# Kernel optimization log

Hardware: AMD Instinct MI355X
Metric: run time of the kernel (lower is better)

## Reference

```python
import jax, jax.numpy as jnp
import numpy as np

E = 768
H = 12
DK = E // H
B = 4
S = 2048
EPS = 1e-5


def setup_inputs() -> dict:
    key = jax.random.key(0)
    ks = jax.random.split(key, 8)
    # xavier_uniform bound for square [E, E] weight
    bound = float(np.sqrt(6.0 / (E + E)))
    def xavier(k):
        return jax.random.uniform(k, (E, E), jnp.float32, -bound, bound)
    return {
        "query": jax.random.normal(ks[0], (B, S, E), jnp.float32),
        "key": jax.random.normal(ks[1], (B, S, E), jnp.float32),
        "value": jax.random.normal(ks[2], (B, S, E), jnp.float32),
        "enc_attn_mask": jax.random.randint(ks[3], (B, S, S), 0, 2).astype(bool),
        "Wq": xavier(ks[4]),
        "Wk": xavier(ks[5]),
        "Wv": xavier(ks[6]),
        "Wo": xavier(ks[7]),
    }


def reference(query, key, value, enc_attn_mask, Wq, Wk, Wv, Wo):
    b, s, _ = query.shape
    # projections (nn.Linear: y = x @ W.T), split heads -> [b, h, s, dk]
    Q = (query @ Wq.T).reshape(b, s, H, DK).transpose(0, 2, 1, 3)
    K = (key @ Wk.T).reshape(b, s, H, DK).transpose(0, 2, 1, 3)
    V = (value @ Wv.T).reshape(b, s, H, DK).transpose(0, 2, 1, 3)
    # scaled dot-product attention with boolean mask (True -> -1e9)
    scores = jnp.einsum("bhqd,bhkd->bhqk", Q, K) / np.sqrt(DK).astype(np.float32)
    scores = jnp.where(enc_attn_mask[:, None, :, :], jnp.float32(-1e9), scores)
    attn = jax.nn.softmax(scores, axis=-1)
    context = jnp.einsum("bhqk,bhkd->bhqd", attn, V)
    context = context.transpose(0, 2, 1, 3).reshape(b, s, E)
    out = context @ Wo.T + query  # residual
    # fresh nn.LayerNorm(E): weight=1, bias=0, eps=1e-5
    mean = jnp.mean(out, axis=-1, keepdims=True)
    var = jnp.var(out, axis=-1, keepdims=True)
    return (out - mean) * jax.lax.rsqrt(var + EPS)
```

## Files before the change

### kernel.cpp

```cpp
#include <hip/hip_runtime.h>
#include <stdint.h>
#include <stddef.h>

#define HN   12
#define SN   2048
#define EN   768
#define DKN  64
#define BATCH 4
#define MROWS 8192

typedef short bf16x8 __attribute__((ext_vector_type(8)));
typedef float f32x4 __attribute__((ext_vector_type(4)));

__device__ __forceinline__ unsigned short f2bf(float f) {
  union { float f; unsigned u; } x; x.f = f;
  unsigned r = x.u + 0x7fffu + ((x.u >> 16) & 1u);
  return (unsigned short)(r >> 16);
}

#if __has_builtin(__builtin_amdgcn_cvt_pk_bf16_f32)
typedef __bf16 bf16v2 __attribute__((ext_vector_type(2)));
__device__ __forceinline__ unsigned pk_bf16(float a, float b) {
  union { bf16v2 v; unsigned u; } c;
  c.v = __builtin_amdgcn_cvt_pk_bf16_f32(a, b);
  return c.u;
}
#else
__device__ __forceinline__ unsigned pk_bf16(float a, float b) {
  return (unsigned)f2bf(a) | ((unsigned)f2bf(b) << 16);
}
#endif

#define GLD_LDS16(gptr, lptr) \
  __builtin_amdgcn_global_load_lds((const __attribute__((address_space(1))) void*)(gptr), \
                                   (__attribute__((address_space(3))) void*)(lptr), 16, 0, 0)

#define NBIG4 1572864
#define NW4   147456
__global__ __launch_bounds__(256) void cvt_all(const float* __restrict__ q,
                                               const float* __restrict__ k,
                                               const float* __restrict__ v,
                                               const float* __restrict__ wq,
                                               const float* __restrict__ wk,
                                               const float* __restrict__ wv,
                                               const float* __restrict__ wo,
                                               unsigned short* __restrict__ dst) {
  const int i = blockIdx.x * 256 + threadIdx.x;
  const float* src;
  int off;
  if (i < 3 * NBIG4) {
    const int r = i / NBIG4;
    src = (r == 0) ? q : (r == 1) ? k : v;
    off = i - r * NBIG4;
  } else {
    const int j = i - 3 * NBIG4;
    const int r = j / NW4;
    src = (r == 0) ? wq : (r == 1) ? wk : (r == 2) ? wv : wo;
    off = j - r * NW4;
  }
  float4 val = ((const float4*)src)[off];
  ushort4 o;
  o.x = f2bf(val.x); o.y = f2bf(val.y); o.z = f2bf(val.z); o.w = f2bf(val.w);
  ((ushort4*)dst)[i] = o;
}

__global__ __launch_bounds__(256) void mask_pack(const int* __restrict__ mask,
                                                 unsigned long long* __restrict__ out) {
  const int row = (blockIdx.x * 256 + threadIdx.x) >> 6;
  const int lane = threadIdx.x & 63;
  const int* mrow = mask + (size_t)row * SN;
  unsigned long long* orow = out + (size_t)row * 32;
  for (int kt = 0; kt < 32; ++kt) {
    int v = mrow[kt * 64 + lane];
    unsigned long long bm = __ballot(v != 0);
    if (lane == 0) orow[kt] = bm;
  }
}

__global__ __launch_bounds__(256) void gemm_qkv(const unsigned short* __restrict__ Xb,
                                                const unsigned short* __restrict__ Wb,
                                                unsigned short* __restrict__ Ob,
                                                float qscale) {
  __shared__ unsigned short As[128 * 32];
  __shared__ unsigned short Bs[128 * 32];
  const int tid  = threadIdx.x;
  const int wave = tid >> 6;
  const int lane = tid & 63;
  const int quad = lane >> 4;
  const int l16  = lane & 15;
  const int bm = blockIdx.x;
  const int bn = blockIdx.y;
  const int z  = blockIdx.z;
  const int wm = wave & 1;
  const int wn = wave >> 1;

  const unsigned short* X = Xb + (size_t)z * MROWS * EN;
  const unsigned short* W = Wb + (size_t)z * EN * EN;
  unsigned short* O = Ob + (size_t)z * MROWS * EN;

  f32x4 acc[4][4] = {};
  const int srow = lane >> 2;
  const int schk = lane & 3;

  for (int bk = 0; bk < 24; ++bk) {
    __syncthreads();
#pragma unroll
    for (int r = 0; r < 2; ++r) {
      const int rowblk = r * 64 + wave * 16;
      GLD_LDS16(X + (size_t)(bm * 128 + rowblk + srow) * EN + bk * 32 + schk * 8,
                As + rowblk * 32);
      GLD_LDS16(W + (size_t)(bn * 128 + rowblk + srow) * EN + bk * 32 + schk * 8,
                Bs + rowblk * 32);
    }
    __syncthreads();

    bf16x8 af[4], bfr[4];
#pragma unroll
    for (int mt = 0; mt < 4; ++mt)
      af[mt] = *(const bf16x8*)&As[(wm * 64 + mt * 16 + l16) * 32 + quad * 8];
#pragma unroll
    for (int nt = 0; nt < 4; ++nt)
      bfr[nt] = *(const bf16x8*)&Bs[(wn * 64 + nt * 16 + l16) * 32 + quad * 8];
#pragma unroll
    for (int mt = 0; mt < 4; ++mt)
#pragma unroll
      for (int nt = 0; nt < 4; ++nt)
        acc[mt][nt] = __builtin_amdgcn_mfma_f32_16x16x32_bf16(af[mt], bfr[nt], acc[mt][nt], 0, 0, 0);
  }

  const int m0 = bm * 128 + wm * 64;
  const int n0 = bn * 128 + wn * 64;
  const float scale = (z == 0) ? qscale : 1.0f;

  if (z < 2) {
#pragma unroll
    for (int mt = 0; mt < 4; ++mt) {
#pragma unroll
      for (int nt = 0; nt < 4; ++nt) {
        const int n = n0 + nt * 16 + l16;
        const int h = n >> 6, d = n & 63;
#pragma unroll
        for (int r = 0; r < 4; ++r) {
          const int m = m0 + mt * 16 + quad * 4 + r;
          const int b = m >> 11, s = m & 2047;
          O[((size_t)(b * HN + h) * SN + s) * DKN + d] = f2bf(acc[mt][nt][r] * scale);
        }
      }
    }
  } else {
#pragma unroll
    for (int mt = 0; mt < 4; ++mt) {
#pragma unroll
      for (int nt = 0; nt < 4; ++nt) {
        const int n = n0 + nt * 16 + l16;
        const int h = n >> 6, d = n & 63;
        const int m = m0 + mt * 16 + quad * 4;
        const int b = m >> 11, s = m & 2047;
        ushort4 pk;
        pk.x = f2bf(acc[mt][nt][0]);
        pk.y = f2bf(acc[mt][nt][1]);
        pk.z = f2bf(acc[mt][nt][2]);
        pk.w = f2bf(acc[mt][nt][3]);
        *(ushort4*)&O[((size_t)(b * HN + h) * DKN + d) * SN + s] = pk;
      }
    }
  }
}

__global__ __launch_bounds__(256) void gemm_out(const unsigned short* __restrict__ X,
                                                const unsigned short* __restrict__ W,
                                                float* __restrict__ O,
                                                const float* __restrict__ residual) {
  __shared__ unsigned short As[128 * 32];
  __shared__ unsigned short Bs[128 * 32];
  const int tid  = threadIdx.x;
  const int wave = tid >> 6;
  const int lane = tid & 63;
  const int quad = lane >> 4;
  const int l16  = lane & 15;
  const int bm = blockIdx.x;
  const int bn = blockIdx.y;
  const int wm = wave & 1;
  const int wn = wave >> 1;

  f32x4 acc[4][4] = {};
  const int srow = lane >> 2;
  const int schk = lane & 3;

  for (int bk = 0; bk < 24; ++bk) {
    __syncthreads();
#pragma unroll
    for (int r = 0; r < 2; ++r) {
      const int rowblk = r * 64 + wave * 16;
      GLD_LDS16(X + (size_t)(bm * 128 + rowblk + srow) * EN + bk * 32 + schk * 8,
                As + rowblk * 32);
      GLD_LDS16(W + (size_t)(bn * 128 + rowblk + srow) * EN + bk * 32 + schk * 8,
                Bs + rowblk * 32);
    }
    __syncthreads();

    bf16x8 af[4], bfr[4];
#pragma unroll
    for (int mt = 0; mt < 4; ++mt)
      af[mt] = *(const bf16x8*)&As[(wm * 64 + mt * 16 + l16) * 32 + quad * 8];
#pragma unroll
    for (int nt = 0; nt < 4; ++nt)
      bfr[nt] = *(const bf16x8*)&Bs[(wn * 64 + nt * 16 + l16) * 32 + quad * 8];
#pragma unroll
    for (int mt = 0; mt < 4; ++mt)
#pragma unroll
      for (int nt = 0; nt < 4; ++nt)
        acc[mt][nt] = __builtin_amdgcn_mfma_f32_16x16x32_bf16(af[mt], bfr[nt], acc[mt][nt], 0, 0, 0);
  }

  const int m0 = bm * 128 + wm * 64;
  const int n0 = bn * 128 + wn * 64;
#pragma unroll
  for (int mt = 0; mt < 4; ++mt) {
#pragma unroll
    for (int nt = 0; nt < 4; ++nt) {
      const int n = n0 + nt * 16 + l16;
#pragma unroll
      for (int r = 0; r < 4; ++r) {
        const int m = m0 + mt * 16 + quad * 4 + r;
        const size_t idx = (size_t)m * EN + n;
        O[idx] = acc[mt][nt][r] + residual[idx];
      }
    }
  }
}

__global__ __launch_bounds__(256, 4) void attn_kernel(const unsigned short* __restrict__ Q,
                                                      const unsigned short* __restrict__ K,
                                                      const unsigned short* __restrict__ Vt,
                                                      const unsigned* __restrict__ Mbits32,
                                                      unsigned short* __restrict__ Ctx) {
  __shared__ __align__(16) unsigned char LDSBUF[64 * 68 * 4];
  __shared__ float lpart[2][2][16];
  unsigned short* Ks = (unsigned short*)LDSBUF;
  unsigned short* Vs = (unsigned short*)(LDSBUF + 8192);
  float* Cmb = (float*)LDSBUF;

  const int tid  = threadIdx.x;
  const int wave = tid >> 6, lane = tid & 63;
  const int quad = lane >> 4, l16 = lane & 15;
  const int qhalf = wave >> 1, kh = wave & 1;
  const int qt = blockIdx.x, bh = blockIdx.y;
  const int b = bh / HN, h = bh - b * HN;

  const unsigned short* Qp = Q + (size_t)bh * SN * DKN;
  const unsigned short* Kp = K + (size_t)bh * SN * DKN;
  const unsigned short* Vp = Vt + (size_t)bh * DKN * SN;

  const int srow = lane >> 3;
  const int schk = lane & 7;
  const int swsrc = (schk ^ srow) * 8;
  const int c0 = (quad ^ (l16 & 7)) * 8;
  const int cv = (((kh << 2) + quad) ^ (l16 & 7)) * 8;
  const int shq = 31 - quad * 8;

  const int pw = wave * 8 + srow;
  const int yk = (((pw >> 2) & 3) << 3) + ((pw >> 4) << 2) + (pw & 3);

  bf16x8 bq[2][2];
#pragma unroll
  for (int qg = 0; qg < 2; ++qg) {
    const int R = qt * 64 + qhalf * 32 + qg * 16 + l16;
    bq[qg][0] = *(const bf16x8*)(Qp + (size_t)R * DKN + quad * 8);
    bq[qg][1] = *(const bf16x8*)(Qp + (size_t)R * DKN + 32 + quad * 8);
  }

  const unsigned* M0 = Mbits32 + ((size_t)(b * SN + qt * 64 + qhalf * 32 + l16)) * 64 + kh;

  f32x4 o_acc[2][4] = {};
  f32x4 o_l[2] = {};
  bf16x8 ones;
#pragma unroll
  for (int i = 0; i < 8; ++i) ones[i] = (short)0x3F80;

  for (int kt = 0; kt < 32; ++kt) {
    __syncthreads();
    GLD_LDS16(Kp + (size_t)(kt * 64 + yk) * DKN + swsrc,              Ks + (wave * 8) * 64);
    GLD_LDS16(Kp + (size_t)(kt * 64 + 32 + yk) * DKN + swsrc,         Ks + (32 + wave * 8) * 64);
    GLD_LDS16(Vp + (size_t)(wave * 8 + srow) * SN + kt * 64 + swsrc,      Vs + (wave * 8) * 64);
    GLD_LDS16(Vp + (size_t)(32 + wave * 8 + srow) * SN + kt * 64 + swsrc, Vs + (32 + wave * 8) * 64);
    const unsigned m0w = M0[kt * 2];
    const unsigned m1w = M0[kt * 2 + 16 * 64];
    __syncthreads();

    bf16x8 ak[2][2];
#pragma unroll
    for (int mt = 0; mt < 2; ++mt) {
      const int base = (kh * 32 + mt * 16 + l16) * 64;
      ak[mt][0] = *(const bf16x8*)&Ks[base + c0];
      ak[mt][1] = *(const bf16x8*)&Ks[base + (c0 ^ 32)];
    }

    f32x4 st[2][2];
#pragma unroll
    for (int qg = 0; qg < 2; ++qg)
#pragma unroll
      for (int mt = 0; mt < 2; ++mt) {
        f32x4 c = {};
        c = __builtin_amdgcn_mfma_f32_16x16x32_bf16(ak[mt][0], bq[qg][0], c, 0, 0, 0);
        c = __builtin_amdgcn_mfma_f32_16x16x32_bf16(ak[mt][1], bq[qg][1], c, 0, 0, 0);
        st[qg][mt] = c;
      }

    bf16x8 av[4];
#pragma unroll
    for (int dt = 0; dt < 4; ++dt)
      av[dt] = *(const bf16x8*)&Vs[(dt * 16 + l16) * 64 + cv];

#pragma unroll
    for (int qg = 0; qg < 2; ++qg) {
      const unsigned w = qg ? m1w : m0w;
      float p[8];
#pragma unroll
      for (int mt = 0; mt < 2; ++mt)
#pragma unroll
        for (int r = 0; r < 4; ++r) {
          const float sv = ((int)(w << (shq - mt * 4 - r)) < 0) ? -1e9f : st[qg][mt][r];
          p[mt * 4 + r] = __builtin_exp2f(sv);
        }
      union { unsigned u[4]; bf16x8 v; } pk;
      pk.u[0] = pk_bf16(p[0], p[1]);
      pk.u[1] = pk_bf16(p[2], p[3]);
      pk.u[2] = pk_bf16(p[4], p[5]);
      pk.u[3] = pk_bf16(p[6], p[7]);
      o_l[qg] = __builtin_amdgcn_mfma_f32_16x16x32_bf16(ones, pk.v, o_l[qg], 0, 0, 0);
#pragma unroll
      for (int dt = 0; dt < 4; ++dt)
        o_acc[qg][dt] = __builtin_amdgcn_mfma_f32_16x16x32_bf16(av[dt], pk.v, o_acc[qg][dt], 0, 0, 0);
    }
  }

  __syncthreads();
  if (kh == 1) {
#pragma unroll
    for (int qg = 0; qg < 2; ++qg) {
#pragma unroll
      for (int dt = 0; dt < 4; ++dt)
        *(f32x4*)&Cmb[(qhalf * 32 + qg * 16 + l16) * 68 + dt * 16 + quad * 4] = o_acc[qg][dt];
      if (quad == 0) lpart[qhalf][qg][l16] = o_l[qg][0];
    }
  }
  __syncthreads();
  if (kh == 0) {
#pragma unroll
    for (int qg = 0; qg < 2; ++qg) {
      const float l = o_l[qg][0] + lpart[qhalf][qg][l16];
      const float inv = 1.0f / l;
      const int R = qt * 64 + qhalf * 32 + qg * 16 + l16;
      unsigned short* Crow = Ctx + (size_t)(b * SN + R) * EN + h * 64;
#pragma unroll
      for (int dt = 0; dt < 4; ++dt) {
        const f32x4 part = *(const f32x4*)&Cmb[(qhalf * 32 + qg * 16 + l16) * 68 + dt * 16 + quad * 4];
        ushort4 wst;
        wst.x = f2bf((o_acc[qg][dt][0] + part[0]) * inv);
        wst.y = f2bf((o_acc[qg][dt][1] + part[1]) * inv);
        wst.z = f2bf((o_acc[qg][dt][2] + part[2]) * inv);
        wst.w = f2bf((o_acc[qg][dt][3] + part[3]) * inv);
        *(ushort4*)&Crow[dt * 16 + quad * 4] = wst;
      }
    }
  }
}

__global__ __launch_bounds__(256) void ln_kernel(const float* __restrict__ X,
                                                 float* __restrict__ Y) {
  const int row = blockIdx.x;
  const int t = threadIdx.x;
  const float* xr = X + (size_t)row * EN;
  float v[3];
  float s = 0.f, ss = 0.f;
#pragma unroll
  for (int i = 0; i < 3; ++i) {
    v[i] = xr[t + i * 256];
    s += v[i];
    ss += v[i] * v[i];
  }
#pragma unroll
  for (int off = 1; off < 64; off <<= 1) {
    s += __shfl_xor(s, off, 64);
    ss += __shfl_xor(ss, off, 64);
  }
  __shared__ float ws_s[4], ws_q[4];
  const int wave = t >> 6, lane = t & 63;
  if (lane == 0) { ws_s[wave] = s; ws_q[wave] = ss; }
  __syncthreads();
  s = ws_s[0] + ws_s[1] + ws_s[2] + ws_s[3];
  ss = ws_q[0] + ws_q[1] + ws_q[2] + ws_q[3];
  const float mean = s * (1.0f / EN);
  const float var = ss * (1.0f / EN) - mean * mean;
  const float rstd = rsqrtf(var + 1e-5f);
  float* yr = Y + (size_t)row * EN;
#pragma unroll
  for (int i = 0; i < 3; ++i) yr[t + i * 256] = (v[i] - mean) * rstd;
}

extern "C" void kernel_launch(void* const* d_in, const int* in_sizes, int n_in,
                              void* d_out, int out_size, void* d_ws, size_t ws_size,
                              hipStream_t stream) {
  (void)in_sizes; (void)n_in; (void)out_size; (void)ws_size;
  const float* query = (const float*)d_in[0];
  const float* key_i = (const float*)d_in[1];
  const float* value = (const float*)d_in[2];
  const int*   mask  = (const int*)d_in[3];
  const float* Wq = (const float*)d_in[4];
  const float* Wk = (const float*)d_in[5];
  const float* Wv = (const float*)d_in[6];
  const float* Wo = (const float*)d_in[7];

  const size_t NBIG = (size_t)MROWS * EN;
  const size_t NW   = (size_t)EN * EN;

  unsigned short* Xq16 = (unsigned short*)d_ws;
  unsigned short* Wq16 = Xq16 + 3 * NBIG;
  unsigned short* Wo16 = Wq16 + 3 * NW;
  unsigned short* Q16  = Wo16 + NW;
  unsigned short* K16  = Q16 + NBIG;
  unsigned short* Vt16 = K16 + NBIG;
  unsigned short* Ctx16 = Vt16 + NBIG;
  float* OutF = (float*)(Ctx16 + NBIG);
  unsigned long long* Mbits = (unsigned long long*)OutF;

  mask_pack<<<MROWS / 4, 256, 0, stream>>>(mask, Mbits);

  const int ncvt = 3 * NBIG4 + 4 * NW4;
  cvt_all<<<ncvt / 256, 256, 0, stream>>>(query, key_i, value, Wq, Wk, Wv, Wo, Xq16);

  gemm_qkv<<<dim3(MROWS / 128, EN / 128, 3), 256, 0, stream>>>(
      Xq16, Wq16, Q16, 0.125f * 1.44269504088896f);

  attn_kernel<<<dim3(SN / 64, BATCH * HN), 256, 0, stream>>>(
      Q16, K16, Vt16, (const unsigned*)Mbits, Ctx16);

  gemm_out<<<dim3(MROWS / 128, EN / 128), 256, 0, stream>>>(Ctx16, Wo16, OutF, query);

  ln_kernel<<<MROWS, 256, 0, stream>>>(OutF, (float*)d_out);
}
```

Baseline: 375.6 us.

## Load K and V tiles directly from global into registers, dropping LDS staging

The attention kernel no longer stages each 64-key K/V tile into shared memory with global-to-LDS loads and two block barriers per iteration. Each lane now reads its MFMA operand fragments straight from global memory, relying on L2/L1 caching since waves in the block and across query tiles reread the same K/V rows. This removes the per-iteration barriers and LDS traffic but duplicates global loads across waves and exposes load latency without explicit prefetch.

```diff
diff --git a/kernel.cpp b/kernel.cpp
--- a/kernel.cpp
+++ b/kernel.cpp
@@ -235,11 +235,8 @@
                                                       const unsigned short* __restrict__ Vt,
                                                       const unsigned* __restrict__ Mbits32,
                                                       unsigned short* __restrict__ Ctx) {
-  __shared__ __align__(16) unsigned char LDSBUF[64 * 68 * 4];
+  __shared__ __align__(16) float Cmb[64 * 68];
   __shared__ float lpart[2][2][16];
-  unsigned short* Ks = (unsigned short*)LDSBUF;
-  unsigned short* Vs = (unsigned short*)(LDSBUF + 8192);
-  float* Cmb = (float*)LDSBUF;
 
   const int tid  = threadIdx.x;
   const int wave = tid >> 6, lane = tid & 63;
@@ -252,15 +249,9 @@
   const unsigned short* Kp = K + (size_t)bh * SN * DKN;
   const unsigned short* Vp = Vt + (size_t)bh * DKN * SN;
 
-  const int srow = lane >> 3;
-  const int schk = lane & 7;
-  const int swsrc = (schk ^ srow) * 8;
-  const int c0 = (quad ^ (l16 & 7)) * 8;
-  const int cv = (((kh << 2) + quad) ^ (l16 & 7)) * 8;
-  const int shq = 31 - quad * 8;
-
-  const int pw = wave * 8 + srow;
-  const int yk = (((pw >> 2) & 3) << 3) + ((pw >> 4) << 2) + (pw & 3);
+  const int krow_base = kh * 32 + ((l16 >> 2) << 3) + (l16 & 3);
+  const unsigned short* Kl = Kp + (size_t)krow_base * DKN + quad * 8;
+  const unsigned short* Vl = Vp + (size_t)l16 * SN + kh * 32 + quad * 8;
 
   bf16x8 bq[2][2];
 #pragma unroll
@@ -278,23 +269,23 @@
 #pragma unroll
   for (int i = 0; i < 8; ++i) ones[i] = (short)0x3F80;
 
+  const int shq = 31 - quad * 8;
+
   for (int kt = 0; kt < 32; ++kt) {
-    __syncthreads();
-    GLD_LDS16(Kp + (size_t)(kt * 64 + yk) * DKN + swsrc,              Ks + (wave * 8) * 64);
-    GLD_LDS16(Kp + (size_t)(kt * 64 + 32 + yk) * DKN + swsrc,         Ks + (32 + wave * 8) * 64);
-    GLD_LDS16(Vp + (size_t)(wave * 8 + srow) * SN + kt * 64 + swsrc,      Vs + (wave * 8) * 64);
-    GLD_LDS16(Vp + (size_t)(32 + wave * 8 + srow) * SN + kt * 64 + swsrc, Vs + (32 + wave * 8) * 64);
+    const size_t ko = (size_t)(kt * 64) * DKN;
+    bf16x8 ak[2][2];
+#pragma unroll
+    for (int mt = 0; mt < 2; ++mt) {
+      const unsigned short* kr = Kl + ko + (size_t)(mt * 4) * DKN;
+      ak[mt][0] = *(const bf16x8*)(kr);
+      ak[mt][1] = *(const bf16x8*)(kr + 32);
+    }
+    bf16x8 av[4];
+#pragma unroll
+    for (int dt = 0; dt < 4; ++dt)
+      av[dt] = *(const bf16x8*)(Vl + (size_t)(dt * 16) * SN + kt * 64);
     const unsigned m0w = M0[kt * 2];
     const unsigned m1w = M0[kt * 2 + 16 * 64];
-    __syncthreads();
-
-    bf16x8 ak[2][2];
-#pragma unroll
-    for (int mt = 0; mt < 2; ++mt) {
-      const int base = (kh * 32 + mt * 16 + l16) * 64;
-      ak[mt][0] = *(const bf16x8*)&Ks[base + c0];
-      ak[mt][1] = *(const bf16x8*)&Ks[base + (c0 ^ 32)];
-    }
 
     f32x4 st[2][2];
 #pragma unroll
@@ -306,11 +297,6 @@
         c = __builtin_amdgcn_mfma_f32_16x16x32_bf16(ak[mt][1], bq[qg][1], c, 0, 0, 0);
         st[qg][mt] = c;
       }
-
-    bf16x8 av[4];
-#pragma unroll
-    for (int dt = 0; dt < 4; ++dt)
-      av[dt] = *(const bf16x8*)&Vs[(dt * 16 + l16) * 64 + cv];
 
 #pragma unroll
     for (int qg = 0; qg < 2; ++qg) {
```

New measurement: 496.6 us. 32.2% more time.

## Double-buffer K/V tiles in LDS and mask probabilities with bitwise AND

Applied to the files above, without the earlier changes.

Splits the attention key loop into a stage/compute pair over two LDS buffers, so the async global-to-LDS loads of the next K/V tile are issued before computing on the current tile. This hides load latency behind MFMA work and needs one barrier per tile instead of two back-to-back barriers. The mask is now applied by AND-ing the exp2 result with a sign-extended bit mask instead of selecting -1e9 before the exponent. LDS use rises to 32 KB per block, which may limit occupancy, and the mask word loads now sit inside the compute body.

```diff
diff --git a/kernel.cpp b/kernel.cpp
--- a/kernel.cpp
+++ b/kernel.cpp
@@ -235,10 +235,10 @@
                                                       const unsigned short* __restrict__ Vt,
                                                       const unsigned* __restrict__ Mbits32,
                                                       unsigned short* __restrict__ Ctx) {
-  __shared__ __align__(16) unsigned char LDSBUF[64 * 68 * 4];
+  __shared__ __align__(16) unsigned char LDSBUF[32768];
   __shared__ float lpart[2][2][16];
-  unsigned short* Ks = (unsigned short*)LDSBUF;
-  unsigned short* Vs = (unsigned short*)(LDSBUF + 8192);
+  unsigned short* Ks0 = (unsigned short*)LDSBUF;
+  unsigned short* Ks1 = (unsigned short*)(LDSBUF + 16384);
   float* Cmb = (float*)LDSBUF;
 
   const int tid  = threadIdx.x;
@@ -278,22 +278,25 @@
 #pragma unroll
   for (int i = 0; i < 8; ++i) ones[i] = (short)0x3F80;
 
-  for (int kt = 0; kt < 32; ++kt) {
-    __syncthreads();
-    GLD_LDS16(Kp + (size_t)(kt * 64 + yk) * DKN + swsrc,              Ks + (wave * 8) * 64);
-    GLD_LDS16(Kp + (size_t)(kt * 64 + 32 + yk) * DKN + swsrc,         Ks + (32 + wave * 8) * 64);
-    GLD_LDS16(Vp + (size_t)(wave * 8 + srow) * SN + kt * 64 + swsrc,      Vs + (wave * 8) * 64);
-    GLD_LDS16(Vp + (size_t)(32 + wave * 8 + srow) * SN + kt * 64 + swsrc, Vs + (32 + wave * 8) * 64);
-    const unsigned m0w = M0[kt * 2];
-    const unsigned m1w = M0[kt * 2 + 16 * 64];
-    __syncthreads();
+  auto stage = [&](unsigned short* ks, int t) {
+    unsigned short* vs = ks + 4096;
+    GLD_LDS16(Kp + (size_t)(t * 64 + yk) * DKN + swsrc,              ks + (wave * 8) * 64);
+    GLD_LDS16(Kp + (size_t)(t * 64 + 32 + yk) * DKN + swsrc,         ks + (32 + wave * 8) * 64);
+    GLD_LDS16(Vp + (size_t)(wave * 8 + srow) * SN + t * 64 + swsrc,      vs + (wave * 8) * 64);
+    GLD_LDS16(Vp + (size_t)(32 + wave * 8 + srow) * SN + t * 64 + swsrc, vs + (32 + wave * 8) * 64);
+  };
+
+  auto body = [&](const unsigned short* ks, int t) {
+    const unsigned short* vs = ks + 4096;
+    const unsigned m0w = M0[t * 2];
+    const unsigned m1w = M0[t * 2 + 16 * 64];
 
     bf16x8 ak[2][2];
 #pragma unroll
     for (int mt = 0; mt < 2; ++mt) {
       const int base = (kh * 32 + mt * 16 + l16) * 64;
-      ak[mt][0] = *(const bf16x8*)&Ks[base + c0];
-      ak[mt][1] = *(const bf16x8*)&Ks[base + (c0 ^ 32)];
+      ak[mt][0] = *(const bf16x8*)&ks[base + c0];
+      ak[mt][1] = *(const bf16x8*)&ks[base + (c0 ^ 32)];
     }
 
     f32x4 st[2][2];
@@ -310,18 +313,20 @@
     bf16x8 av[4];
 #pragma unroll
     for (int dt = 0; dt < 4; ++dt)
-      av[dt] = *(const bf16x8*)&Vs[(dt * 16 + l16) * 64 + cv];
+      av[dt] = *(const bf16x8*)&vs[(dt * 16 + l16) * 64 + cv];
 
 #pragma unroll
     for (int qg = 0; qg < 2; ++qg) {
-      const unsigned w = qg ? m1w : m0w;
+      const unsigned wn = ~(qg ? m1w : m0w);
       float p[8];
 #pragma unroll
       for (int mt = 0; mt < 2; ++mt)
 #pragma unroll
         for (int r = 0; r < 4; ++r) {
-          const float sv = ((int)(w << (shq - mt * 4 - r)) < 0) ? -1e9f : st[qg][mt][r];
-          p[mt * 4 + r] = __builtin_exp2f(sv);
+          union { float f; unsigned u; } pu;
+          pu.f = __builtin_exp2f(st[qg][mt][r]);
+          pu.u &= (unsigned)((int)(wn << (shq - mt * 4 - r)) >> 31);
+          p[mt * 4 + r] = pu.f;
         }
       union { unsigned u[4]; bf16x8 v; } pk;
       pk.u[0] = pk_bf16(p[0], p[1]);
@@ -333,6 +338,16 @@
       for (int dt = 0; dt < 4; ++dt)
         o_acc[qg][dt] = __builtin_amdgcn_mfma_f32_16x16x32_bf16(av[dt], pk.v, o_acc[qg][dt], 0, 0, 0);
     }
+  };
+
+  stage(Ks0, 0);
+  for (int kt2 = 0; kt2 < 16; ++kt2) {
+    __syncthreads();
+    stage(Ks1, kt2 * 2 + 1);
+    body(Ks0, kt2 * 2);
+    __syncthreads();
+    if (kt2 < 15) stage(Ks0, kt2 * 2 + 2);
+    body(Ks1, kt2 * 2 + 1);
   }
 
   __syncthreads();
```

Result: slower. 385.1 us (+2.5%).
